# Kernel tuning notes

Hardware: AMD Instinct MI355X
Metric: run time of the kernel (lower is better)

The kernel has to match this reference:

```python
import jax, jax.numpy as jnp
import numpy as np

B, P, S, D = 16, 512, 1024, 1024
H_FULL, H_LIGHT = 16, 8


def _mha(q, k, v, w_in, b_in, w_out, b_out, nh):
    # PyTorch nn.MultiheadAttention (batch_first=True), dropout=0 (eval).
    d = q.shape[-1]
    hd = d // nh
    wq, wk, wv = jnp.split(w_in, 3, axis=0)
    bq, bk, bv = jnp.split(b_in, 3, axis=0)

    def proj(x, w, b):
        return (x @ w.T + b).reshape(x.shape[0], x.shape[1], nh, hd)

    qh = proj(q, wq, bq)  # [B,Lq,H,hd]
    kh = proj(k, wk, bk)  # [B,Lk,H,hd]
    vh = proj(v, wv, bv)
    scale = 1.0 / jnp.sqrt(jnp.asarray(hd, q.dtype))
    scores = jnp.einsum('bqhd,bkhd->bhqk', qh, kh) * scale
    attn = jax.nn.softmax(scores, axis=-1)
    o = jnp.einsum('bhqk,bkhd->bqhd', attn, vh).reshape(q.shape[0], q.shape[1], d)
    out = o @ w_out.T + b_out
    return out, attn.mean(axis=1)  # avg weights over heads (torch default)


def _ln(x, g, b, eps=1e-5):
    mu = x.mean(-1, keepdims=True)
    var = ((x - mu) ** 2).mean(-1, keepdims=True)
    return (x - mu) / jnp.sqrt(var + eps) * g + b


def setup_inputs() -> dict:
    key = jax.random.key(0)
    ks = jax.random.split(key, 16)
    w = 0.02
    inp = {
        'proto': jax.random.normal(ks[0], (B, P, D), jnp.float32),
        'img_features': jax.random.normal(ks[1], (B, S, D), jnp.float32),
        'cross_w_in': jax.random.normal(ks[2], (3 * D, D), jnp.float32) * w,
        'cross_b_in': jnp.zeros((3 * D,), jnp.float32),
        'cross_w_out': jax.random.normal(ks[3], (D, D), jnp.float32) * w,
        'cross_b_out': jnp.zeros((D,), jnp.float32),
        'self_w_in': jax.random.normal(ks[4], (3 * D, D), jnp.float32) * w,
        'self_b_in': jnp.zeros((3 * D,), jnp.float32),
        'self_w_out': jax.random.normal(ks[5], (D, D), jnp.float32) * w,
        'self_b_out': jnp.zeros((D,), jnp.float32),
        'light_w_in': jax.random.normal(ks[6], (3 * D, D), jnp.float32) * w,
        'light_b_in': jnp.zeros((3 * D,), jnp.float32),
        'light_w_out': jax.random.normal(ks[7], (D, D), jnp.float32) * w,
        'light_b_out': jnp.zeros((D,), jnp.float32),
        'norm1_g': jnp.ones((D,), jnp.float32), 'norm1_b': jnp.zeros((D,), jnp.float32),
        'norm2_g': jnp.ones((D,), jnp.float32), 'norm2_b': jnp.zeros((D,), jnp.float32),
        'norm3_g': jnp.ones((D,), jnp.float32), 'norm3_b': jnp.zeros((D,), jnp.float32),
        'gate_w1': jax.random.normal(ks[8], (D, 3 * D), jnp.float32) * w,
        'gate_b1': jnp.zeros((D,), jnp.float32),
        'gate_w2': jax.random.normal(ks[9], (3, D), jnp.float32) * w,
        'gate_b2': jnp.zeros((3,), jnp.float32),
    }
    return inp


def reference(proto, img_features,
              cross_w_in, cross_b_in, cross_w_out, cross_b_out,
              self_w_in, self_b_in, self_w_out, self_b_out,
              light_w_in, light_b_in, light_w_out, light_b_out,
              norm1_g, norm1_b, norm2_g, norm2_b, norm3_g, norm3_b,
              gate_w1, gate_b1, gate_w2, gate_b2):
    cross_raw, attn_w = _mha(proto, img_features, img_features,
                             cross_w_in, cross_b_in, cross_w_out, cross_b_out, H_FULL)
    cross_out = _ln(proto + cross_raw, norm1_g, norm1_b)
    self_raw, _ = _mha(cross_out, cross_out, cross_out,
                       self_w_in, self_b_in, self_w_out, self_b_out, H_FULL)
    self_out = _ln(cross_out + self_raw, norm2_g, norm2_b)
    light_raw, _ = _mha(self_out, self_out, self_out,
                        light_w_in, light_b_in, light_w_out, light_b_out, H_LIGHT)
    light_out = _ln(self_out + light_raw, norm3_g, norm3_b)
    gate_in = jnp.concatenate([cross_out, self_out, light_out], axis=-1)  # [B,P,3D]
    h = jax.nn.gelu(gate_in @ gate_w1.T + gate_b1, approximate=False)
    gate_w = jax.nn.softmax(h @ gate_w2.T + gate_b2, axis=-1)  # [B,P,3]
    updated = (gate_w[..., 0:1] * cross_out
               + gate_w[..., 1:2] * self_out
               + gate_w[..., 2:3] * light_out)
    return updated, attn_w
```

## Files before the change

### kernel.cpp

```cpp
#include <hip/hip_runtime.h>
#include <hip/hip_bf16.h>

typedef __hip_bfloat16 bf16;
typedef __attribute__((ext_vector_type(8))) short short8;
typedef __attribute__((ext_vector_type(4))) float f32x4;

#define BD 16
#define PD 512
#define SD 1024
#define DD 1024

#define GLDS16(gp, lp)                                              \
  __builtin_amdgcn_global_load_lds(                                 \
      (const __attribute__((address_space(1))) void*)(gp),          \
      (__attribute__((address_space(3))) void*)(lp), 16, 0, 0)

__global__ __launch_bounds__(256) void f2b(const float* __restrict__ in,
                                           bf16* __restrict__ out, int n)
{
  int i = (blockIdx.x * 256 + threadIdx.x) * 4;
  if (i < n) {
    float4 v = *(const float4*)(in + i);
    out[i + 0] = __float2bfloat16(v.x);
    out[i + 1] = __float2bfloat16(v.y);
    out[i + 2] = __float2bfloat16(v.z);
    out[i + 3] = __float2bfloat16(v.w);
  }
}

__global__ __launch_bounds__(256) void gemm_nt(
    const bf16* __restrict__ A, int lda,
    const bf16* __restrict__ W, int ldw,
    const float* __restrict__ bias,
    bf16* __restrict__ C, int ldc,
    int K, int gelu)
{
  __shared__ bf16 As[128 * 32];
  __shared__ bf16 Bs[128 * 32];

  const int t = threadIdx.x;
  const int lane = t & 63, wv = t >> 6;
  const int m0 = blockIdx.y * 128;
  const int n0 = blockIdx.x * 128;
  const int rl = lane & 15, qd = lane >> 4;

  f32x4 acc[4][4];
  for (int i = 0; i < 4; i++)
    for (int j = 0; j < 4; j++)
      acc[i][j] = (f32x4){0.f, 0.f, 0.f, 0.f};

  const bf16* Ag = A + (size_t)(m0 + (t >> 2)) * lda + (t & 3) * 8;
  const bf16* Wg = W + (size_t)(n0 + (t >> 2)) * ldw + (t & 3) * 8;
  const size_t a_half = (size_t)64 * lda, w_half = (size_t)64 * ldw;
  bf16* As0 = As + wv * 512;
  bf16* As1 = As + 2048 + wv * 512;
  bf16* Bs0 = Bs + wv * 512;
  bf16* Bs1 = Bs + 2048 + wv * 512;

  const int mw = (wv >> 1) * 64, nw = (wv & 1) * 64;

  for (int k0 = 0; k0 < K; k0 += 32) {
    GLDS16(Ag + k0, As0);
    GLDS16(Ag + a_half + k0, As1);
    GLDS16(Wg + k0, Bs0);
    GLDS16(Wg + w_half + k0, Bs1);
    __syncthreads();

    short8 a[4], b[4];
#pragma unroll
    for (int i = 0; i < 4; i++)
      a[i] = *(const short8*)&As[(mw + i * 16 + rl) * 32 + qd * 8];
#pragma unroll
    for (int j = 0; j < 4; j++)
      b[j] = *(const short8*)&Bs[(nw + j * 16 + rl) * 32 + qd * 8];
#pragma unroll
    for (int i = 0; i < 4; i++)
#pragma unroll
      for (int j = 0; j < 4; j++)
        acc[i][j] = __builtin_amdgcn_mfma_f32_16x16x32_bf16(a[i], b[j], acc[i][j], 0, 0, 0);
    __syncthreads();
  }

  for (int i = 0; i < 4; i++) {
    const int row = m0 + mw + i * 16 + qd * 4;
    for (int j = 0; j < 4; j++) {
      const int col = n0 + nw + j * 16 + rl;
      const float bv = bias[col];
      for (int r = 0; r < 4; r++) {
        float v = acc[i][j][r] + bv;
        if (gelu) v = 0.5f * v * (1.0f + erff(v * 0.70710678118654752f));
        C[(size_t)(row + r) * ldc + col] = __float2bfloat16(v);
      }
    }
  }
}

__global__ void transpose_v(const bf16* __restrict__ V, int ldv, int voff,
                            bf16* __restrict__ Vt, int L, int H, int hd)
{
  __shared__ float tile[32][33];
  const int bh = blockIdx.z;
  const int b = bh / H, h = bh % H;
  const int d0 = blockIdx.x * 32, s0 = blockIdx.y * 32;
  const int tx = threadIdx.x, ty = threadIdx.y;
  tile[ty][tx] = __bfloat162float(V[(size_t)(b * L + s0 + ty) * ldv + voff + h * hd + d0 + tx]);
  __syncthreads();
  Vt[(size_t)((b * H + h) * hd + d0 + ty) * L + s0 + tx] = __float2bfloat16(tile[tx][ty]);
}

template<int HD, bool STATS>
__global__ __launch_bounds__(256) void flash_attn(
    const bf16* __restrict__ Q, int ldq, int qoff,
    const bf16* __restrict__ Km, int ldk, int koff,
    const bf16* __restrict__ Vt,
    bf16* __restrict__ O, int ldo, int ooff,
    float* __restrict__ linv_out,
    int H, int Lq, int Lk, float scale)
{
  constexpr int KK = HD / 32;
  constexpr int NO = HD / 16;
  __shared__ __align__(16) __hip_bfloat16 pl[4][2][2][16][32];

  const int lane = threadIdx.x & 63, wv = threadIdx.x >> 6;
  const int rl = lane & 15, qd = lane >> 4;
  const int b = blockIdx.z, h = blockIdx.y;
  const int q0 = blockIdx.x * 128 + wv * 32;

  short8 qf[2][KK];
  for (int mt = 0; mt < 2; ++mt)
    for (int kk = 0; kk < KK; ++kk)
      qf[mt][kk] = *(const short8*)(Q + (size_t)(b * Lq + q0 + mt * 16 + rl) * ldq
                                      + qoff + h * HD + kk * 32 + qd * 8);

  const bf16* Kb = Km + (size_t)b * Lk * ldk + koff + h * HD + qd * 8;
  const bf16* Vb = Vt + (size_t)(b * H + h) * HD * Lk + qd * 8;

  float ls[2][4];
  for (int mt = 0; mt < 2; mt++)
    for (int r = 0; r < 4; r++) ls[mt][r] = 0.f;
  f32x4 oacc[2][NO];
  for (int mt = 0; mt < 2; mt++)
    for (int ni = 0; ni < NO; ni++) oacc[mt][ni] = (f32x4){0.f, 0.f, 0.f, 0.f};

  const int nS32 = Lk / 32;
  for (int i = 0; i < nS32; i++) {
    const int s0 = i * 32;
    for (int f = 0; f < 2; f++) {
      short8 kf[KK];
#pragma unroll
      for (int kk = 0; kk < KK; kk++)
        kf[kk] = *(const short8*)(Kb + (size_t)(s0 + f * 16 + rl) * ldk + kk * 32);
#pragma unroll
      for (int mt = 0; mt < 2; mt++) {
        f32x4 sc = (f32x4){0.f, 0.f, 0.f, 0.f};
#pragma unroll
        for (int kk = 0; kk < KK; kk++)
          sc = __builtin_amdgcn_mfma_f32_16x16x32_bf16(qf[mt][kk], kf[kk], sc, 0, 0, 0);
        for (int r = 0; r < 4; r++) {
          float p = __expf(sc[r] * scale);
          ls[mt][r] += p;
          pl[wv][i & 1][mt][qd * 4 + r][f * 16 + rl] = __float2bfloat16(p);
        }
      }
    }
    asm volatile("s_waitcnt lgkmcnt(0)" ::: "memory");
    short8 vf[NO];
#pragma unroll
    for (int ni = 0; ni < NO; ni++)
      vf[ni] = *(const short8*)(Vb + (size_t)(ni * 16 + rl) * Lk + s0);
#pragma unroll
    for (int mt = 0; mt < 2; mt++) {
      short8 pa = *(const short8*)&pl[wv][i & 1][mt][rl][qd * 8];
#pragma unroll
      for (int ni = 0; ni < NO; ni++)
        oacc[mt][ni] = __builtin_amdgcn_mfma_f32_16x16x32_bf16(pa, vf[ni], oacc[mt][ni], 0, 0, 0);
    }
  }

  float rinv[2][4];
  for (int mt = 0; mt < 2; mt++)
    for (int r = 0; r < 4; r++) {
      float v = ls[mt][r];
      for (int o = 1; o < 16; o <<= 1) v += __shfl_xor(v, o);
      rinv[mt][r] = 1.0f / v;
    }

  if (STATS) {
    if (rl == 0)
      for (int mt = 0; mt < 2; mt++)
        for (int r = 0; r < 4; r++)
          linv_out[((size_t)b * H + h) * Lq + q0 + mt * 16 + qd * 4 + r] = rinv[mt][r];
  }

  for (int mt = 0; mt < 2; mt++)
    for (int ni = 0; ni < NO; ni++)
      for (int r = 0; r < 4; r++)
        O[(size_t)(b * Lq + q0 + mt * 16 + qd * 4 + r) * ldo + ooff + h * HD + ni * 16 + rl]
            = __float2bfloat16(oacc[mt][ni][r] * rinv[mt][r]);
}

template<int HD>
__global__ __launch_bounds__(256) void probs_mean(
    const bf16* __restrict__ Q, int ldq, int qoff,
    const bf16* __restrict__ Km, int ldk, int koff,
    const float* __restrict__ linv, float* __restrict__ out_att,
    int H, int Lq, int Lk, float scale)
{
  constexpr int KK = HD / 32;
  const int lane = threadIdx.x & 63, wv = threadIdx.x >> 6;
  const int rl = lane & 15, qd = lane >> 4;
  const int b = blockIdx.z;
  const int q0 = blockIdx.x * 128 + wv * 32;
  const int s0 = blockIdx.y * 32;
  const float hs = 1.0f / 16.0f;

  f32x4 am[2][2];
  for (int mt = 0; mt < 2; mt++)
    for (int f = 0; f < 2; f++) am[mt][f] = (f32x4){0.f, 0.f, 0.f, 0.f};

  const bf16* Qb  = Q  + (size_t)(b * Lq + q0) * ldq + qoff + qd * 8;
  const bf16* Kb0 = Km + (size_t)(b * Lk + s0) * ldk + koff + qd * 8;
  const float* lb = linv + (size_t)b * H * Lq + q0 + qd * 4;

  for (int h = 0; h < H; h++) {
    short8 qf[2][KK], kf[2][KK];
#pragma unroll
    for (int mt = 0; mt < 2; mt++)
#pragma unroll
      for (int kk = 0; kk < KK; kk++)
        qf[mt][kk] = *(const short8*)(Qb + (size_t)(mt * 16 + rl) * ldq + h * HD + kk * 32);
#pragma unroll
    for (int f = 0; f < 2; f++)
#pragma unroll
      for (int kk = 0; kk < KK; kk++)
        kf[f][kk] = *(const short8*)(Kb0 + (size_t)(f * 16 + rl) * ldk + h * HD + kk * 32);
    float li[2][4];
#pragma unroll
    for (int mt = 0; mt < 2; mt++)
#pragma unroll
      for (int r = 0; r < 4; r++)
        li[mt][r] = lb[(size_t)h * Lq + mt * 16 + r];
#pragma unroll
    for (int mt = 0; mt < 2; mt++)
#pragma unroll
      for (int f = 0; f < 2; f++) {
        f32x4 sc = (f32x4){0.f, 0.f, 0.f, 0.f};
#pragma unroll
        for (int kk = 0; kk < KK; kk++)
          sc = __builtin_amdgcn_mfma_f32_16x16x32_bf16(qf[mt][kk], kf[f][kk], sc, 0, 0, 0);
#pragma unroll
        for (int r = 0; r < 4; r++)
          am[mt][f][r] += __expf(sc[r] * scale) * li[mt][r];
      }
  }

#pragma unroll
  for (int mt = 0; mt < 2; mt++)
#pragma unroll
    for (int f = 0; f < 2; f++)
#pragma unroll
      for (int r = 0; r < 4; r++)
        out_att[(size_t)(b * Lq + q0 + mt * 16 + qd * 4 + r) * Lk + s0 + f * 16 + rl]
            = am[mt][f][r] * hs;
}

template<bool XF32>
__global__ __launch_bounds__(256) void add_ln(
    const void* __restrict__ Xv, int ldx, int xoff,
    const bf16* __restrict__ Y,
    const float* __restrict__ g, const float* __restrict__ bb,
    bf16* __restrict__ out, int ldo, int ooff)
{
  const int row = blockIdx.x, t = threadIdx.x;
  const bf16* yr = Y + (size_t)row * 1024;
  float v[4], s = 0.f, s2 = 0.f;
  for (int i = 0; i < 4; i++) {
    int c = t * 4 + i;
    float xv;
    if (XF32) xv = ((const float*)Xv)[(size_t)row * ldx + xoff + c];
    else      xv = __bfloat162float(((const bf16*)Xv)[(size_t)row * ldx + xoff + c]);
    v[i] = xv + __bfloat162float(yr[c]);
    s += v[i]; s2 += v[i] * v[i];
  }
  __shared__ float red[2][4];
  for (int o = 32; o >= 1; o >>= 1) { s += __shfl_down(s, o); s2 += __shfl_down(s2, o); }
  const int wv = t >> 6, lane = t & 63;
  if (lane == 0) { red[0][wv] = s; red[1][wv] = s2; }
  __syncthreads();
  s  = red[0][0] + red[0][1] + red[0][2] + red[0][3];
  s2 = red[1][0] + red[1][1] + red[1][2] + red[1][3];
  const float mean = s * (1.0f / 1024.f);
  const float var = s2 * (1.0f / 1024.f) - mean * mean;
  const float rstd = rsqrtf(var + 1e-5f);
  for (int i = 0; i < 4; i++) {
    int c = t * 4 + i;
    float o = (v[i] - mean) * rstd * g[c] + bb[c];
    out[(size_t)row * ldo + ooff + c] = __float2bfloat16(o);
  }
}

__global__ __launch_bounds__(256) void gate_kernel(
    const bf16* __restrict__ Hb, const bf16* __restrict__ G,
    const float* __restrict__ w2, const float* __restrict__ b2,
    float* __restrict__ out)
{
  const int row = blockIdx.x, t = threadIdx.x;
  const bf16* hr = Hb + (size_t)row * 1024;
  float d0 = 0.f, d1 = 0.f, d2 = 0.f;
  for (int i = 0; i < 4; i++) {
    int c = t * 4 + i;
    float hv = __bfloat162float(hr[c]);
    d0 += hv * w2[c];
    d1 += hv * w2[1024 + c];
    d2 += hv * w2[2048 + c];
  }
  __shared__ float red[3][4];
  for (int o = 32; o >= 1; o >>= 1) {
    d0 += __shfl_down(d0, o); d1 += __shfl_down(d1, o); d2 += __shfl_down(d2, o);
  }
  const int wv = t >> 6, lane = t & 63;
  if (lane == 0) { red[0][wv] = d0; red[1][wv] = d1; red[2][wv] = d2; }
  __syncthreads();
  float l0 = red[0][0] + red[0][1] + red[0][2] + red[0][3] + b2[0];
  float l1 = red[1][0] + red[1][1] + red[1][2] + red[1][3] + b2[1];
  float l2 = red[2][0] + red[2][1] + red[2][2] + red[2][3] + b2[2];
  float mm = fmaxf(l0, fmaxf(l1, l2));
  float e0 = __expf(l0 - mm), e1 = __expf(l1 - mm), e2 = __expf(l2 - mm);
  float inv = 1.f / (e0 + e1 + e2);
  float g0 = e0 * inv, g1 = e1 * inv, g2 = e2 * inv;
  const bf16* gr = G + (size_t)row * 3072;
  for (int i = 0; i < 4; i++) {
    int c = t * 4 + i;
    float o = g0 * __bfloat162float(gr[c]) + g1 * __bfloat162float(gr[1024 + c])
            + g2 * __bfloat162float(gr[2048 + c]);
    out[(size_t)row * 1024 + c] = o;
  }
}

extern "C" void kernel_launch(void* const* d_in, const int* in_sizes, int n_in,
                              void* d_out, int out_size, void* d_ws, size_t ws_size,
                              hipStream_t stream)
{
  const float* proto = (const float*)d_in[0];
  const float* img   = (const float*)d_in[1];
  const float* c_wi  = (const float*)d_in[2];
  const float* c_bi  = (const float*)d_in[3];
  const float* c_wo  = (const float*)d_in[4];
  const float* c_bo  = (const float*)d_in[5];
  const float* s_wi  = (const float*)d_in[6];
  const float* s_bi  = (const float*)d_in[7];
  const float* s_wo  = (const float*)d_in[8];
  const float* s_bo  = (const float*)d_in[9];
  const float* l_wi  = (const float*)d_in[10];
  const float* l_bi  = (const float*)d_in[11];
  const float* l_wo  = (const float*)d_in[12];
  const float* l_bo  = (const float*)d_in[13];
  const float* n1g = (const float*)d_in[14]; const float* n1b = (const float*)d_in[15];
  const float* n2g = (const float*)d_in[16]; const float* n2b = (const float*)d_in[17];
  const float* n3g = (const float*)d_in[18]; const float* n3b = (const float*)d_in[19];
  const float* gw1 = (const float*)d_in[20]; const float* gb1 = (const float*)d_in[21];
  const float* gw2 = (const float*)d_in[22]; const float* gb2 = (const float*)d_in[23];

  float* out_upd = (float*)d_out;
  float* out_att = out_upd + (size_t)BD * PD * DD;

  char* ws = (char*)d_ws;
  bf16* WB = (bf16*)ws;
  bf16* w_cwi = WB + 0;
  bf16* w_cwo = WB + 3145728;
  bf16* w_swi = WB + 4194304;
  bf16* w_swo = WB + 7340032;
  bf16* w_lwi = WB + 8388608;
  bf16* w_lwo = WB + 11534336;
  bf16* w_gw1 = WB + 12582912;

  int bc = 16;
  while (bc > 1 && 31457280ull + (size_t)bc * 16777216ull > ws_size) bc >>= 1;

  char* pool = ws + 31457280;
  bf16*  Pb    = (bf16*)pool;
  bf16*  Ib    = (bf16*)(pool + (size_t)1048576 * bc);
  bf16*  G     = (bf16*)(pool + (size_t)3145728 * bc);
  bf16*  Vg    = (bf16*)(pool + (size_t)6291456 * bc);
  float* linvb = (float*)(pool + (size_t)6291456 * bc);
  bf16*  Bq    = (bf16*)(pool + (size_t)8388608 * bc);
  bf16*  Vt    = (bf16*)(pool + (size_t)11534336 * bc);
  bf16*  Qc    = (bf16*)(pool + (size_t)13631488 * bc);
  bf16*  AO    = (bf16*)(pool + (size_t)14680064 * bc);
  bf16*  OP    = (bf16*)(pool + (size_t)15728640 * bc);

  const dim3 blk(256);

  f2b<<<dim3(3072), blk, 0, stream>>>(c_wi, w_cwi, 3145728);
  f2b<<<dim3(1024), blk, 0, stream>>>(c_wo, w_cwo, 1048576);
  f2b<<<dim3(3072), blk, 0, stream>>>(s_wi, w_swi, 3145728);
  f2b<<<dim3(1024), blk, 0, stream>>>(s_wo, w_swo, 1048576);
  f2b<<<dim3(3072), blk, 0, stream>>>(l_wi, w_lwi, 3145728);
  f2b<<<dim3(1024), blk, 0, stream>>>(l_wo, w_lwo, 1048576);
  f2b<<<dim3(3072), blk, 0, stream>>>(gw1, w_gw1, 3145728);

  for (int b0 = 0; b0 < BD; b0 += bc) {
    const float* proto_c = proto + (size_t)b0 * PD * DD;
    const float* img_c   = img + (size_t)b0 * SD * DD;
    float* out_upd_c = out_upd + (size_t)b0 * PD * DD;
    float* out_att_c = out_att + (size_t)b0 * PD * SD;
    const int MP = bc * PD;
    const int MS = bc * SD;

    f2b<<<dim3(MP), blk, 0, stream>>>(proto_c, Pb, MP * DD);
    f2b<<<dim3(MS), blk, 0, stream>>>(img_c, Ib, MS * DD);

    gemm_nt<<<dim3(8, MP / 128), blk, 0, stream>>>(Pb, 1024, w_cwi, 1024, c_bi,
                                                   Qc, 1024, 1024, 0);
    gemm_nt<<<dim3(8, MS / 128), blk, 0, stream>>>(Ib, 1024, w_cwi + (size_t)1024 * 1024, 1024,
                                                   c_bi + 1024, Bq, 1024, 1024, 0);
    gemm_nt<<<dim3(8, MS / 128), blk, 0, stream>>>(Ib, 1024, w_cwi + (size_t)2048 * 1024, 1024,
                                                   c_bi + 2048, Vg, 1024, 1024, 0);
    transpose_v<<<dim3(2, 32, bc * 16), dim3(32, 32), 0, stream>>>(Vg, 1024, 0, Vt, 1024, 16, 64);
    flash_attn<64, true><<<dim3(4, 16, bc), blk, 0, stream>>>(
        Qc, 1024, 0, Bq, 1024, 0, Vt, AO, 1024, 0, linvb, 16, PD, SD, 0.125f);
    probs_mean<64><<<dim3(4, SD / 32, bc), blk, 0, stream>>>(
        Qc, 1024, 0, Bq, 1024, 0, linvb, out_att_c, 16, PD, SD, 0.125f);
    gemm_nt<<<dim3(8, MP / 128), blk, 0, stream>>>(AO, 1024, w_cwo, 1024, c_bo, OP, 1024, 1024, 0);
    add_ln<true><<<dim3(MP), blk, 0, stream>>>(proto_c, 1024, 0, OP, n1g, n1b, G, 3072, 0);

    gemm_nt<<<dim3(24, MP / 128), blk, 0, stream>>>(G, 3072, w_swi, 1024, s_bi, Bq, 3072, 1024, 0);
    transpose_v<<<dim3(2, 16, bc * 16), dim3(32, 32), 0, stream>>>(Bq, 3072, 2048, Vt, 512, 16, 64);
    flash_attn<64, false><<<dim3(4, 16, bc), blk, 0, stream>>>(
        Bq, 3072, 0, Bq, 3072, 1024, Vt, AO, 1024, 0, nullptr, 16, PD, PD, 0.125f);
    gemm_nt<<<dim3(8, MP / 128), blk, 0, stream>>>(AO, 1024, w_swo, 1024, s_bo, OP, 1024, 1024, 0);
    add_ln<false><<<dim3(MP), blk, 0, stream>>>(G, 3072, 0, OP, n2g, n2b, G, 3072, 1024);

    gemm_nt<<<dim3(24, MP / 128), blk, 0, stream>>>(G + 1024, 3072, w_lwi, 1024, l_bi,
                                                    Bq, 3072, 1024, 0);
    transpose_v<<<dim3(4, 16, bc * 8), dim3(32, 32), 0, stream>>>(Bq, 3072, 2048, Vt, 512, 8, 128);
    flash_attn<128, false><<<dim3(4, 8, bc), blk, 0, stream>>>(
        Bq, 3072, 0, Bq, 3072, 1024, Vt, AO, 1024, 0, nullptr, 8, PD, PD,
        0.08838834764831845f);
    gemm_nt<<<dim3(8, MP / 128), blk, 0, stream>>>(AO, 1024, w_lwo, 1024, l_bo, OP, 1024, 1024, 0);
    add_ln<false><<<dim3(MP), blk, 0, stream>>>(G, 3072, 1024, OP, n3g, n3b, G, 3072, 2048);

    gemm_nt<<<dim3(8, MP / 128), blk, 0, stream>>>(G, 3072, w_gw1, 3072, gb1, Qc, 1024, 3072, 1);
    gate_kernel<<<dim3(MP), blk, 0, stream>>>(Qc, G, gw2, gb2, out_upd_c);
  }
}
```

Baseline: 1.456 ms.

## Triple-buffer GEMM LDS tiles with async global-to-LDS prefetch

Turns the bf16 NT GEMM main loop from a load-sync-compute-sync pattern into a three-stage ring buffer. Loads for tile k+2 are issued before computing tile k, with s_waitcnt vmcnt and a single barrier per iteration replacing the two __syncthreads. The aim is to hide global memory latency behind MFMA work. In exchange, LDS use per block triples, which may lower occupancy, and correctness depends on the vmcnt counting and barrier ordering being right.

```diff
diff --git a/kernel.cpp b/kernel.cpp
--- a/kernel.cpp
+++ b/kernel.cpp
@@ -35,8 +35,8 @@
     bf16* __restrict__ C, int ldc,
     int K, int gelu)
 {
-  __shared__ bf16 As[128 * 32];
-  __shared__ bf16 Bs[128 * 32];
+  __shared__ bf16 As[3][128 * 32];
+  __shared__ bf16 Bs[3][128 * 32];
 
   const int t = threadIdx.x;
   const int lane = t & 63, wv = t >> 6;
@@ -52,34 +52,49 @@
   const bf16* Ag = A + (size_t)(m0 + (t >> 2)) * lda + (t & 3) * 8;
   const bf16* Wg = W + (size_t)(n0 + (t >> 2)) * ldw + (t & 3) * 8;
   const size_t a_half = (size_t)64 * lda, w_half = (size_t)64 * ldw;
-  bf16* As0 = As + wv * 512;
-  bf16* As1 = As + 2048 + wv * 512;
-  bf16* Bs0 = Bs + wv * 512;
-  bf16* Bs1 = Bs + 2048 + wv * 512;
+  const int lo = wv * 512;
 
   const int mw = (wv >> 1) * 64, nw = (wv & 1) * 64;
 
-  for (int k0 = 0; k0 < K; k0 += 32) {
-    GLDS16(Ag + k0, As0);
-    GLDS16(Ag + a_half + k0, As1);
-    GLDS16(Wg + k0, Bs0);
-    GLDS16(Wg + w_half + k0, Bs1);
-    __syncthreads();
-
+  const int nt = K >> 5;
+
+#define STAGE(buf, k0)                          \
+  do {                                          \
+    GLDS16(Ag + (k0), &As[buf][lo]);            \
+    GLDS16(Ag + a_half + (k0), &As[buf][2048 + lo]); \
+    GLDS16(Wg + (k0), &Bs[buf][lo]);            \
+    GLDS16(Wg + w_half + (k0), &Bs[buf][2048 + lo]); \
+  } while (0)
+
+  STAGE(0, 0);
+  STAGE(1, 32);
+
+  int cur = 0, pf = 2;
+  for (int tt = 0; tt < nt; ++tt) {
+    if (tt + 1 < nt) asm volatile("s_waitcnt vmcnt(4)" ::: "memory");
+    else             asm volatile("s_waitcnt vmcnt(0)" ::: "memory");
+    __builtin_amdgcn_s_barrier();
+    if (tt + 2 < nt) STAGE(pf, (tt + 2) * 32);
+
+    const bf16* Ac = As[cur];
+    const bf16* Bc = Bs[cur];
     short8 a[4], b[4];
 #pragma unroll
     for (int i = 0; i < 4; i++)
-      a[i] = *(const short8*)&As[(mw + i * 16 + rl) * 32 + qd * 8];
+      a[i] = *(const short8*)&Ac[(mw + i * 16 + rl) * 32 + qd * 8];
 #pragma unroll
     for (int j = 0; j < 4; j++)
-      b[j] = *(const short8*)&Bs[(nw + j * 16 + rl) * 32 + qd * 8];
+      b[j] = *(const short8*)&Bc[(nw + j * 16 + rl) * 32 + qd * 8];
 #pragma unroll
     for (int i = 0; i < 4; i++)
 #pragma unroll
       for (int j = 0; j < 4; j++)
         acc[i][j] = __builtin_amdgcn_mfma_f32_16x16x32_bf16(a[i], b[j], acc[i][j], 0, 0, 0);
-    __syncthreads();
-  }
+
+    cur = (cur == 2) ? 0 : cur + 1;
+    pf  = (pf == 2) ? 0 : pf + 1;
+  }
+#undef STAGE
 
   for (int i = 0; i < 4; i++) {
     const int row = m0 + mw + i * 16 + qd * 4;
```

Result: faster. 1.397 ms (-4.0%).
